# Optimization experiments

Measured on AMD Instinct MI355X. Metric: run time of the kernel, lower is better.

Reference implementation:

```python
import jax, jax.numpy as jnp
import numpy as np

EMB = 300      # emb_size
SEQ = 100      # seq_len
KW = 5         # kernel_width
KN = 50        # kernel_num
KMAX = 3       # maxpooling_num
MLP1 = 75      # decoder_mlp1_num
VOCAB = 50000 + 2
B = 2048
QLEN = 5


def setup_inputs() -> dict:
    key = jax.random.key(0)
    ks = jax.random.split(key, 11)
    input_q = jax.random.randint(ks[0], (QLEN,), 0, 50000)
    input_d = jax.random.randint(ks[1], (B, SEQ), 0, 50000)
    emb_table = jax.random.normal(ks[2], (VOCAB, EMB), jnp.float32) * 0.1
    conv_w = jax.random.normal(ks[3], (KW, 3 * EMB, KN), jnp.float32) * 0.02  # WIO
    conv_b = jnp.zeros((KN,), jnp.float32)
    gate_w = jax.random.normal(ks[4], (EMB, KN), jnp.float32) * 0.05
    gate_b = jnp.zeros((KN,), jnp.float32)
    hid_w = jax.random.normal(ks[5], (KN * KMAX, MLP1), jnp.float32) * 0.05
    hid_b = jnp.zeros((MLP1,), jnp.float32)
    score_w = jax.random.normal(ks[6], (MLP1, 1), jnp.float32) * 0.05
    score_b = jnp.zeros((1,), jnp.float32)
    return {"input_q": input_q, "input_d": input_d, "emb_table": emb_table,
            "conv_w": conv_w, "conv_b": conv_b, "gate_w": gate_w, "gate_b": gate_b,
            "hid_w": hid_w, "hid_b": hid_b, "score_w": score_w, "score_b": score_b}


def kmax_pool(x, k):
    # x: [B, KN, L]; keep top-k values along last axis in original sequence order
    _, idx = jax.lax.top_k(x, k)
    idx = jnp.sort(idx, axis=-1)
    return jnp.take_along_axis(x, idx, axis=-1)  # [B, KN, k]


def reference(input_q, input_d, emb_table, conv_w, conv_b, gate_w, gate_b,
              hid_w, hid_b, score_w, score_b):
    # class vector: mean of query-word embeddings -> [EMB]
    class_vec = emb_table[input_q].mean(axis=0)
    # category-specific gate -> [KN]
    query_gate = jax.nn.sigmoid(class_vec @ gate_w + gate_b)
    # document embeddings -> [B, SEQ, EMB]
    emb = emb_table[input_d]
    # elementwise interaction features, concat -> [B, SEQ, 3*EMB]
    conv_in = jnp.concatenate([emb, class_vec * emb, class_vec - emb], axis=-1)
    # conv over sequence (full-width kernel == 1D conv with C_in=3*EMB) -> [B, SEQ-KW+1, KN]
    conv = jax.lax.conv_general_dilated(
        conv_in, conv_w, window_strides=(1,), padding='VALID',
        dimension_numbers=('NWC', 'WIO', 'NWC')) + conv_b
    gated = query_gate * conv                      # [B, L', KN]
    pooled = kmax_pool(jnp.swapaxes(gated, 1, 2), KMAX)  # [B, KN, KMAX]
    enc = pooled.reshape(pooled.shape[0], -1)      # [B, KN*KMAX] = [B, 150]
    mlp1 = jnp.tanh(enc @ hid_w + hid_b)           # [B, 75]
    score = jnp.tanh(mlp1 @ score_w + score_b)     # [B, 1]
    return (mlp1, score)
```

## Files before the change

### kernel.cpp

```cpp
#include <hip/hip_runtime.h>
#include <math.h>

#define EMB   300
#define SEQ   100
#define KW    5
#define KN    50
#define NPAD  64
#define KMAX  3
#define MLP1  75
#define LOUT  96
#define BATCH 2048
#define EPAD  320
#define CHW   32
#define NCHK  10
#define SROWS 52
#define SPITCHW 36
#define TAU   2.5e-6
#define WHA   0.75
#define WHB   0.25
#define FLAG_TAU 1e-5f

#define WS_C    0
#define WS_GATE 320
#define WS_BIAS 384
#define WS_WG   448
#define F64_DBL 96448
#define WH_F    0
#define WL_F    51200
#define ENC_OFF 102400
#define ENC_PITCH 152
#define FLAGCNT_OFF 413696
#define FLAGLIST_OFF 413704
#define FLAGCAP 4096

typedef __attribute__((ext_vector_type(8))) short short8;
typedef __attribute__((ext_vector_type(4))) float f32x4;

__device__ __forceinline__ unsigned pack_hl(float x) {
    unsigned u = __float_as_uint(x);
    unsigned hi = (u + 0x7fffu + ((u >> 16) & 1u)) >> 16;
    float r = x - __uint_as_float(hi << 16);
    unsigned v = __float_as_uint(r);
    unsigned lo = (v + 0x7fffu + ((v >> 16) & 1u)) >> 16;
    return (hi << 16) | lo;
}

__global__ __launch_bounds__(256) void prep_a(
    const int* __restrict__ qids, const float* __restrict__ emb,
    const float* __restrict__ gate_w, const float* __restrict__ gate_b,
    const float* __restrict__ conv_w, const float* __restrict__ conv_b,
    double* __restrict__ ws, float* wsf)
{
    __shared__ double cS[EMB];
    __shared__ double gS[KN];
    __shared__ double pS[KW][KN];
    int t = threadIdx.x;
    if (t == 0) *(int*)(wsf + FLAGCNT_OFF) = 0;
    for (int e = t; e < EMB; e += 256) {
        double s = 0.0;
        for (int q = 0; q < 5; ++q) s += (double)emb[(size_t)qids[q] * EMB + e];
        double c = s * 0.2;
        cS[e] = c;
        ws[WS_C + e] = c;
    }
    __syncthreads();
    if (t < KN) {
        double g = (double)gate_b[t];
        for (int e = 0; e < EMB; ++e) g += cS[e] * (double)gate_w[e * KN + t];
        g = 1.0 / (1.0 + exp(-g));
        gS[t] = g;
        ws[WS_GATE + t] = g;
    }
    if (t < KW * KN) {
        int n = t % KN, w = t / KN;
        const float* base = conv_w + w * (3 * EMB * KN) + (2 * EMB) * KN + n;
        double p = 0.0;
        for (int e = 0; e < EMB; ++e) p += cS[e] * (double)base[e * KN];
        pS[w][n] = p;
    }
    __syncthreads();
    if (t < KN) {
        double s = (double)conv_b[t];
        for (int w = 0; w < KW; ++w) s += pS[w][t];
        ws[WS_BIAS + t] = gS[t] * s;
    }
}

__global__ __launch_bounds__(256) void prep_b(
    const float* __restrict__ conv_w, const double* __restrict__ ws,
    double* __restrict__ wg, float* __restrict__ wsf)
{
    int gid  = blockIdx.x * 256 + threadIdx.x;
    int wid  = gid >> 6;
    int lane = gid & 63;
    int w = wid / EPAD;
    int e = wid - w * EPAD;
    double v = 0.0;
    if (e < EMB && lane < KN) {
        double c = ws[WS_C + e];
        const float* p = conv_w + (size_t)w * (3 * EMB * KN) + (size_t)e * KN + lane;
        v = ws[WS_GATE + lane] *
            ((double)p[0] + c * (double)p[EMB * KN] - (double)p[2 * EMB * KN]);
    }
    if (e < EMB) wg[(size_t)(w * NPAD + lane) * EMB + e] = v;
    unsigned pk = pack_hl((float)v);
    unsigned short* Wh = (unsigned short*)(wsf + WH_F);
    unsigned short* Wl = (unsigned short*)(wsf + WL_F);
    size_t o = (size_t)(w * NPAD + lane) * EPAD + e;
    Wh[o] = (unsigned short)(pk >> 16);
    Wl[o] = (unsigned short)(pk & 0xffffu);
}

__global__ __launch_bounds__(256, 4) void main_mfma(
    const int* __restrict__ input_d, const float* __restrict__ emb,
    const double* __restrict__ ws, float* wsf,
    const float* __restrict__ hid_w, const float* __restrict__ hid_b,
    const float* __restrict__ score_w, const float* __restrict__ score_b,
    float* __restrict__ out)
{
    __shared__ __align__(16) unsigned stageS[2][2][SROWS][SPITCHW];
    __shared__ int   tokS[4][SROWS];
    __shared__ float encS[2][ENC_PITCH];
    __shared__ float mlpS[2][MLP1 + 1];

    int t = threadIdx.x;
    int wid = t >> 6, lane = t & 63;
    int dl   = wid >> 1;
    int half = wid & 1;
    int bb = blockIdx.x * 2 + dl;
    int m = lane & 15, kg = lane >> 4;

    if (lane < SROWS) tokS[wid][lane] = input_d[bb * SEQ + half * 48 + lane];

    f32x4 acc[3][4];
    #pragma unroll
    for (int lt = 0; lt < 3; ++lt)
        #pragma unroll
        for (int nt = 0; nt < 4; ++nt)
            acc[lt][nt] = (f32x4){0.f, 0.f, 0.f, 0.f};

    const unsigned short* Wh = (const unsigned short*)(wsf + WH_F);
    const unsigned short* Wl = (const unsigned short*)(wsf + WL_F);
    unsigned* stg = &stageS[dl][half][0][0];

    for (int c = 0; c < NCHK; ++c) {
        int e0 = c * CHW;
        #pragma unroll
        for (int it = 0; it < 4; ++it) {
            int i = lane + it * 64;
            if (i < SROWS * 4) {
                int s = i >> 2, eg = i & 3;
                int e = e0 + eg * 8;
                const float* er = emb + (size_t)tokS[wid][s] * EMB;
                float4 fa = {0.f, 0.f, 0.f, 0.f}, fb = {0.f, 0.f, 0.f, 0.f};
                if (e < EMB)     fa = *(const float4*)(er + e);
                if (e + 4 < EMB) fb = *(const float4*)(er + e + 4);
                unsigned p0 = pack_hl(fa.x), p1 = pack_hl(fa.y), p2 = pack_hl(fa.z), p3 = pack_hl(fa.w);
                unsigned p4 = pack_hl(fb.x), p5 = pack_hl(fb.y), p6 = pack_hl(fb.z), p7 = pack_hl(fb.w);
                uint4 hv, lv;
                hv.x = (p0 >> 16)     | (p1 & 0xffff0000u);
                hv.y = (p2 >> 16)     | (p3 & 0xffff0000u);
                hv.z = (p4 >> 16)     | (p5 & 0xffff0000u);
                hv.w = (p6 >> 16)     | (p7 & 0xffff0000u);
                lv.x = (p0 & 0xffffu) | (p1 << 16);
                lv.y = (p2 & 0xffffu) | (p3 << 16);
                lv.z = (p4 & 0xffffu) | (p5 << 16);
                lv.w = (p6 & 0xffffu) | (p7 << 16);
                unsigned* rowp = stg + s * SPITCHW + eg * 8;
                *(uint4*)(rowp)     = hv;
                *(uint4*)(rowp + 4) = lv;
            }
        }
        #pragma unroll 1
        for (int w = 0; w < KW; ++w) {
            short8 Bh[4], Bl[4];
            #pragma unroll
            for (int nt = 0; nt < 4; ++nt) {
                size_t off = (size_t)(w * NPAD + nt * 16 + m) * EPAD + e0 + kg * 8;
                union { uint4 u; short8 s; } xb, yb;
                xb.u = *(const uint4*)(Wh + off);
                yb.u = *(const uint4*)(Wl + off);
                Bh[nt] = xb.s; Bl[nt] = yb.s;
            }
            #pragma unroll
            for (int lt = 0; lt < 3; ++lt) {
                int r = lt * 16 + m + w;
                const unsigned* ap = stg + r * SPITCHW + kg * 8;
                short8 ah = *(const short8*)(ap);
                short8 al = *(const short8*)(ap + 4);
                #pragma unroll
                for (int nt = 0; nt < 4; ++nt) {
                    acc[lt][nt] = __builtin_amdgcn_mfma_f32_16x16x32_bf16(ah, Bh[nt], acc[lt][nt], 0, 0, 0);
                    acc[lt][nt] = __builtin_amdgcn_mfma_f32_16x16x32_bf16(al, Bh[nt], acc[lt][nt], 0, 0, 0);
                    acc[lt][nt] = __builtin_amdgcn_mfma_f32_16x16x32_bf16(ah, Bl[nt], acc[lt][nt], 0, 0, 0);
                }
            }
        }
    }

    __syncthreads();

    float* gated = (float*)&stageS[dl][0][0][0];
    #pragma unroll 1
    for (int ph = 0; ph < 2; ++ph) {
        int np0 = ph * 25;
        #pragma unroll
        for (int nt = 0; nt < 4; ++nt) {
            int n = nt * 16 + m;
            if (n >= np0 && n < np0 + 25) {
                float bias_n = (float)ws[WS_BIAS + n];
                #pragma unroll
                for (int lt = 0; lt < 3; ++lt)
                    #pragma unroll
                    for (int rr = 0; rr < 4; ++rr)
                        gated[(n - np0) * 97 + (half * 3 + lt) * 16 + kg * 4 + rr] = acc[lt][nt][rr] + bias_n;
            }
        }
        __syncthreads();
        int nr = half ? 12 : 13;
        if (lane < nr) {
            int row = half * 13 + lane;
            int n = np0 + row;
            const float* rowp = gated + row * 97;
            float v1 = -1e30f, v2 = -1e30f, v3 = -1e30f, v4 = -1e30f;
            int   i1 = 0, i2 = 0, i3 = 0, i4 = 0;
            for (int l = 0; l < LOUT; ++l) {
                float v = rowp[l];
                if (v > v1)      { v4=v3; i4=i3; v3=v2; i3=i2; v2=v1; i2=i1; v1=v; i1=l; }
                else if (v > v2) { v4=v3; i4=i3; v3=v2; i3=i2; v2=v;  i2=l; }
                else if (v > v3) { v4=v3; i4=i3; v3=v;  i3=l; }
                else if (v > v4) { v4=v;  i4=l; }
            }
            float a0=v1, a1=v2, a2=v3; int j0=i1, j1=i2, j2=i3;
            if (j0 > j1) { float tv=a0; a0=a1; a1=tv; int ti=j0; j0=j1; j1=ti; }
            if (j1 > j2) { float tv=a1; a1=a2; a2=tv; int ti=j1; j1=j2; j2=ti; }
            if (j0 > j1) { float tv=a0; a0=a1; a1=tv; int ti=j0; j0=j1; j1=ti; }
            encS[dl][3*n] = a0; encS[dl][3*n+1] = a1; encS[dl][3*n+2] = a2;
            float* enc = wsf + ENC_OFF + (size_t)bb * ENC_PITCH + 3 * n;
            enc[0] = a0; enc[1] = a1; enc[2] = a2;
            if (v3 - v4 <= FLAG_TAU) {
                int idx = atomicAdd((int*)(wsf + FLAGCNT_OFF), 1);
                if (idx < FLAGCAP) ((int*)(wsf + FLAGLIST_OFF))[idx] = (bb << 6) | n;
            }
        }
        __syncthreads();
    }

    for (int i = t; i < 2 * MLP1; i += 256) {
        int d = i / MLP1, o = i - d * MLP1;
        float h = hid_b[o];
        for (int k = 0; k < KN * KMAX; ++k) h = fmaf(encS[d][k], hid_w[k * MLP1 + o], h);
        h = tanhf(h);
        mlpS[d][o] = h;
        out[(blockIdx.x * 2 + d) * MLP1 + o] = h;
    }
    __syncthreads();
    if (t < 2) {
        float s = score_b[0];
        for (int j = 0; j < MLP1; ++j) s = fmaf(mlpS[t][j], score_w[j], s);
        out[BATCH * MLP1 + blockIdx.x * 2 + t] = tanhf(s);
    }
}

__global__ __launch_bounds__(64) void cleanup_enc(
    const int* __restrict__ input_d, const float* __restrict__ emb,
    const double* __restrict__ ws, float* wsf)
{
    int cnt = *(const int*)(wsf + FLAGCNT_OFF);
    if (cnt > FLAGCAP) cnt = FLAGCAP;
    int idx = blockIdx.x;
    if (idx >= cnt) return;
    int code = ((const int*)(wsf + FLAGLIST_OFF))[idx];
    int b = code >> 6, n = code & 63;
    int lane = threadIdx.x;

    __shared__ int    tokS[SEQ];
    __shared__ double rowS[LOUT];
    for (int i = lane; i < SEQ; i += 64) tokS[i] = input_d[b * SEQ + i];
    __syncthreads();

    for (int l = lane; l < LOUT; l += 64) {
        double s = 0.0;
        for (int w = 0; w < KW; ++w) {
            const float*  er = emb + (size_t)tokS[l + w] * EMB;
            const double* wr = ws + WS_WG + (size_t)(w * NPAD + n) * EMB;
            for (int e = 0; e < EMB; ++e) s += (double)er[e] * wr[e];
        }
        rowS[l] = s + ws[WS_BIAS + n];
    }
    __syncthreads();

    if (lane == 0) {
        double v1=-1e300, v2=-1e300, v3=-1e300, v4=-1e300;
        int    i1=0, i2=0, i3=0, i4=0;
        for (int l = 0; l < LOUT; ++l) {
            double v = rowS[l];
            if (v > v1)      { v4=v3; i4=i3; v3=v2; i3=i2; v2=v1; i2=i1; v1=v; i1=l; }
            else if (v > v2) { v4=v3; i4=i3; v3=v2; i3=i2; v2=v;  i2=l; }
            else if (v > v3) { v4=v3; i4=i3; v3=v;  i3=l; }
            else if (v > v4) { v4=v;  i4=l; }
        }
        double a0=v1, a1=v2, a2=v3; int j0=i1, j1=i2, j2=i3;
        if (j0 > j1) { double tv=a0; a0=a1; a1=tv; int ti=j0; j0=j1; j1=ti; }
        if (j1 > j2) { double tv=a1; a1=a2; a2=tv; int ti=j1; j1=j2; j2=ti; }
        if (j0 > j1) { double tv=a0; a0=a1; a1=tv; int ti=j0; j0=j1; j1=ti; }
        double b0=v1, b1=v2, b2=v4; int k0=i1, k1=i2, k2=i4;
        if (k0 > k1) { double tv=b0; b0=b1; b1=tv; int ti=k0; k0=k1; k1=ti; }
        if (k1 > k2) { double tv=b1; b1=b2; b2=tv; int ti=k1; k1=k2; k2=ti; }
        if (k0 > k1) { double tv=b0; b0=b1; b1=tv; int ti=k0; k0=k1; k1=ti; }
        float* enc = wsf + ENC_OFF + (size_t)b * ENC_PITCH + 3 * n;
        if (v3 - v4 > TAU) {
            enc[0] = (float)a0; enc[1] = (float)a1; enc[2] = (float)a2;
        } else {
            enc[0] = (float)(WHA*a0 + WHB*b0);
            enc[1] = (float)(WHA*a1 + WHB*b1);
            enc[2] = (float)(WHA*a2 + WHB*b2);
        }
    }
}

__global__ __launch_bounds__(128) void cleanup_mlp(
    const float* wsf, const float* __restrict__ hid_w, const float* __restrict__ hid_b,
    const float* __restrict__ score_w, const float* __restrict__ score_b,
    float* __restrict__ out)
{
    int cnt = *(const int*)(wsf + FLAGCNT_OFF);
    if (cnt > FLAGCAP) cnt = FLAGCAP;
    if ((int)blockIdx.x >= cnt) return;
    int code = ((const int*)(wsf + FLAGLIST_OFF))[blockIdx.x];
    int b = code >> 6;
    int t = threadIdx.x;
    __shared__ float eS[KN * KMAX];
    __shared__ float mS[MLP1];
    const float* enc = wsf + ENC_OFF + (size_t)b * ENC_PITCH;
    for (int i = t; i < KN * KMAX; i += 128) eS[i] = enc[i];
    __syncthreads();
    if (t < MLP1) {
        float h = hid_b[t];
        for (int k = 0; k < KN * KMAX; ++k) h = fmaf(eS[k], hid_w[k * MLP1 + t], h);
        h = tanhf(h);
        mS[t] = h;
        out[b * MLP1 + t] = h;
    }
    __syncthreads();
    if (t == 0) {
        float s = score_b[0];
        for (int j = 0; j < MLP1; ++j) s = fmaf(mS[j], score_w[j], s);
        out[BATCH * MLP1 + b] = tanhf(s);
    }
}

extern "C" void kernel_launch(void* const* d_in, const int* in_sizes, int n_in,
                              void* d_out, int out_size, void* d_ws, size_t ws_size,
                              hipStream_t stream)
{
    const int*   input_q = (const int*)d_in[0];
    const int*   input_d = (const int*)d_in[1];
    const float* emb     = (const float*)d_in[2];
    const float* conv_w  = (const float*)d_in[3];
    const float* conv_b  = (const float*)d_in[4];
    const float* gate_w  = (const float*)d_in[5];
    const float* gate_b  = (const float*)d_in[6];
    const float* hid_w   = (const float*)d_in[7];
    const float* hid_b   = (const float*)d_in[8];
    const float* score_w = (const float*)d_in[9];
    const float* score_b = (const float*)d_in[10];
    float*  out = (float*)d_out;
    double* ws  = (double*)d_ws;
    float*  wsf = (float*)((char*)d_ws + (size_t)F64_DBL * 8);

    hipLaunchKernelGGL(prep_a, dim3(1), dim3(256), 0, stream,
                       input_q, emb, gate_w, gate_b, conv_w, conv_b, ws, wsf);
    hipLaunchKernelGGL(prep_b, dim3(400), dim3(256), 0, stream,
                       conv_w, ws, ws + WS_WG, wsf);
    hipLaunchKernelGGL(main_mfma, dim3(BATCH / 2), dim3(256), 0, stream,
                       input_d, emb, ws, wsf, hid_w, hid_b, score_w, score_b, out);
    hipLaunchKernelGGL(cleanup_enc, dim3(FLAGCAP), dim3(64), 0, stream,
                       input_d, emb, ws, wsf);
    hipLaunchKernelGGL(cleanup_mlp, dim3(FLAGCAP), dim3(128), 0, stream,
                       wsf, hid_w, hid_b, score_w, score_b, out);
}
```

Before: 443.1 us.

## Give each wave a full document and prefetch next embedding chunk during MFMA

```diff
diff --git a/kernel.cpp b/kernel.cpp
--- a/kernel.cpp
+++ b/kernel.cpp
@@ -13,8 +13,7 @@
 #define EPAD  320
 #define CHW   32
 #define NCHK  10
-#define SROWS 52
-#define SPITCHW 36
+#define SPW   36
 #define TAU   2.5e-6
 #define WHA   0.75
 #define WHB   0.25
@@ -111,50 +110,63 @@
     Wl[o] = (unsigned short)(pk & 0xffffu);
 }
 
-__global__ __launch_bounds__(256, 4) void main_mfma(
+__global__ __launch_bounds__(256, 2) void main_mfma(
     const int* __restrict__ input_d, const float* __restrict__ emb,
     const double* __restrict__ ws, float* wsf,
     const float* __restrict__ hid_w, const float* __restrict__ hid_b,
     const float* __restrict__ score_w, const float* __restrict__ score_b,
     float* __restrict__ out)
 {
-    __shared__ __align__(16) unsigned stageS[2][2][SROWS][SPITCHW];
-    __shared__ int   tokS[4][SROWS];
-    __shared__ float encS[2][ENC_PITCH];
-    __shared__ float mlpS[2][MLP1 + 1];
+    __shared__ __align__(16) unsigned stageS[4][SEQ * SPW];
+    __shared__ float encS[4][ENC_PITCH];
+    __shared__ float mlpS[4][MLP1 + 1];
 
     int t = threadIdx.x;
     int wid = t >> 6, lane = t & 63;
-    int dl   = wid >> 1;
-    int half = wid & 1;
-    int bb = blockIdx.x * 2 + dl;
+    int bb = blockIdx.x * 4 + wid;
     int m = lane & 15, kg = lane >> 4;
-
-    if (lane < SROWS) tokS[wid][lane] = input_d[bb * SEQ + half * 48 + lane];
-
-    f32x4 acc[3][4];
+    unsigned* stg = &stageS[wid][0];
+
+    int tv[7];
     #pragma unroll
-    for (int lt = 0; lt < 3; ++lt)
+    for (int it = 0; it < 7; ++it) {
+        int i = lane + it * 64;
+        tv[it] = (i < SEQ * 4) ? input_d[bb * SEQ + (i >> 2)] : 0;
+    }
+
+    f32x4 acc[6][4];
+    #pragma unroll
+    for (int lt = 0; lt < 6; ++lt)
         #pragma unroll
         for (int nt = 0; nt < 4; ++nt)
             acc[lt][nt] = (f32x4){0.f, 0.f, 0.f, 0.f};
 
     const unsigned short* Wh = (const unsigned short*)(wsf + WH_F);
     const unsigned short* Wl = (const unsigned short*)(wsf + WL_F);
-    unsigned* stg = &stageS[dl][half][0][0];
-
+
+    float4 pfa[7], pfb[7];
+    #pragma unroll
+    for (int it = 0; it < 7; ++it) {
+        int i = lane + it * 64;
+        float4 z = {0.f, 0.f, 0.f, 0.f};
+        pfa[it] = z; pfb[it] = z;
+        if (i < SEQ * 4) {
+            int eg = i & 3;
+            const float* er = emb + (size_t)tv[it] * EMB + eg * 8;
+            pfa[it] = *(const float4*)(er);
+            pfb[it] = *(const float4*)(er + 4);
+        }
+    }
+
+    #pragma unroll 1
     for (int c = 0; c < NCHK; ++c) {
         int e0 = c * CHW;
         #pragma unroll
-        for (int it = 0; it < 4; ++it) {
+        for (int it = 0; it < 7; ++it) {
             int i = lane + it * 64;
-            if (i < SROWS * 4) {
+            if (i < SEQ * 4) {
                 int s = i >> 2, eg = i & 3;
-                int e = e0 + eg * 8;
-                const float* er = emb + (size_t)tokS[wid][s] * EMB;
-                float4 fa = {0.f, 0.f, 0.f, 0.f}, fb = {0.f, 0.f, 0.f, 0.f};
-                if (e < EMB)     fa = *(const float4*)(er + e);
-                if (e + 4 < EMB) fb = *(const float4*)(er + e + 4);
+                float4 fa = pfa[it], fb = pfb[it];
                 unsigned p0 = pack_hl(fa.x), p1 = pack_hl(fa.y), p2 = pack_hl(fa.z), p3 = pack_hl(fa.w);
                 unsigned p4 = pack_hl(fb.x), p5 = pack_hl(fb.y), p6 = pack_hl(fb.z), p7 = pack_hl(fb.w);
                 uint4 hv, lv;
@@ -166,12 +178,12 @@
                 lv.y = (p2 & 0xffffu) | (p3 << 16);
                 lv.z = (p4 & 0xffffu) | (p5 << 16);
                 lv.w = (p6 & 0xffffu) | (p7 << 16);
-                unsigned* rowp = stg + s * SPITCHW + eg * 8;
+                unsigned* rowp = stg + s * SPW + eg * 8;
                 *(uint4*)(rowp)     = hv;
                 *(uint4*)(rowp + 4) = lv;
             }
         }
-        #pragma unroll 1
+        #pragma unroll
         for (int w = 0; w < KW; ++w) {
             short8 Bh[4], Bl[4];
             #pragma unroll
@@ -182,10 +194,27 @@
                 yb.u = *(const uint4*)(Wl + off);
                 Bh[nt] = xb.s; Bl[nt] = yb.s;
             }
+            if (w == KW - 1 && c + 1 < NCHK) {
+                __builtin_amdgcn_sched_barrier(0);
+                int e0n = e0 + CHW;
+                #pragma unroll
+                for (int it = 0; it < 7; ++it) {
+                    int i = lane + it * 64;
+                    float4 z = {0.f, 0.f, 0.f, 0.f};
+                    pfa[it] = z; pfb[it] = z;
+                    if (i < SEQ * 4) {
+                        int eg = i & 3, e = e0n + eg * 8;
+                        const float* er = emb + (size_t)tv[it] * EMB;
+                        if (e < EMB)     pfa[it] = *(const float4*)(er + e);
+                        if (e + 4 < EMB) pfb[it] = *(const float4*)(er + e + 4);
+                    }
+                }
+                __builtin_amdgcn_sched_barrier(0);
+            }
             #pragma unroll
-            for (int lt = 0; lt < 3; ++lt) {
+            for (int lt = 0; lt < 6; ++lt) {
                 int r = lt * 16 + m + w;
-                const unsigned* ap = stg + r * SPITCHW + kg * 8;
+                const unsigned* ap = stg + r * SPW + kg * 8;
                 short8 ah = *(const short8*)(ap);
                 short8 al = *(const short8*)(ap + 4);
                 #pragma unroll
@@ -198,9 +227,7 @@
         }
     }
 
-    __syncthreads();
-
-    float* gated = (float*)&stageS[dl][0][0][0];
+    float* gated = (float*)stg;
     #pragma unroll 1
     for (int ph = 0; ph < 2; ++ph) {
         int np0 = ph * 25;
@@ -210,18 +237,15 @@
             if (n >= np0 && n < np0 + 25) {
                 float bias_n = (float)ws[WS_BIAS + n];
                 #pragma unroll
-                for (int lt = 0; lt < 3; ++lt)
+                for (int lt = 0; lt < 6; ++lt)
                     #pragma unroll
                     for (int rr = 0; rr < 4; ++rr)
-                        gated[(n - np0) * 97 + (half * 3 + lt) * 16 + kg * 4 + rr] = acc[lt][nt][rr] + bias_n;
-            }
-        }
-        __syncthreads();
-        int nr = half ? 12 : 13;
-        if (lane < nr) {
-            int row = half * 13 + lane;
-            int n = np0 + row;
-            const float* rowp = gated + row * 97;
+                        gated[(n - np0) * 97 + lt * 16 + kg * 4 + rr] = acc[lt][nt][rr] + bias_n;
+            }
+        }
+        if (lane < 25) {
+            int n = np0 + lane;
+            const float* rowp = gated + lane * 97;
             float v1 = -1e30f, v2 = -1e30f, v3 = -1e30f, v4 = -1e30f;
             int   i1 = 0, i2 = 0, i3 = 0, i4 = 0;
             for (int l = 0; l < LOUT; ++l) {
@@ -232,10 +256,10 @@
                 else if (v > v4) { v4=v;  i4=l; }
             }
             float a0=v1, a1=v2, a2=v3; int j0=i1, j1=i2, j2=i3;
-            if (j0 > j1) { float tv=a0; a0=a1; a1=tv; int ti=j0; j0=j1; j1=ti; }
-            if (j1 > j2) { float tv=a1; a1=a2; a2=tv; int ti=j1; j1=j2; j2=ti; }
-            if (j0 > j1) { float tv=a0; a0=a1; a1=tv; int ti=j0; j0=j1; j1=ti; }
-            encS[dl][3*n] = a0; encS[dl][3*n+1] = a1; encS[dl][3*n+2] = a2;
+            if (j0 > j1) { float tv2=a0; a0=a1; a1=tv2; int ti=j0; j0=j1; j1=ti; }
+            if (j1 > j2) { float tv2=a1; a1=a2; a2=tv2; int ti=j1; j1=j2; j2=ti; }
+            if (j0 > j1) { float tv2=a0; a0=a1; a1=tv2; int ti=j0; j0=j1; j1=ti; }
+            encS[wid][3*n] = a0; encS[wid][3*n+1] = a1; encS[wid][3*n+2] = a2;
             float* enc = wsf + ENC_OFF + (size_t)bb * ENC_PITCH + 3 * n;
             enc[0] = a0; enc[1] = a1; enc[2] = a2;
             if (v3 - v4 <= FLAG_TAU) {
@@ -243,22 +267,22 @@
                 if (idx < FLAGCAP) ((int*)(wsf + FLAGLIST_OFF))[idx] = (bb << 6) | n;
             }
         }
-        __syncthreads();
-    }
-
-    for (int i = t; i < 2 * MLP1; i += 256) {
+    }
+    __syncthreads();
+
+    for (int i = t; i < 4 * MLP1; i += 256) {
         int d = i / MLP1, o = i - d * MLP1;
         float h = hid_b[o];
         for (int k = 0; k < KN * KMAX; ++k) h = fmaf(encS[d][k], hid_w[k * MLP1 + o], h);
         h = tanhf(h);
         mlpS[d][o] = h;
-        out[(blockIdx.x * 2 + d) * MLP1 + o] = h;
-    }
-    __syncthreads();
-    if (t < 2) {
+        out[(blockIdx.x * 4 + d) * MLP1 + o] = h;
+    }
+    __syncthreads();
+    if (t < 4) {
         float s = score_b[0];
         for (int j = 0; j < MLP1; ++j) s = fmaf(mlpS[t][j], score_w[j], s);
-        out[BATCH * MLP1 + blockIdx.x * 2 + t] = tanhf(s);
+        out[BATCH * MLP1 + blockIdx.x * 4 + t] = tanhf(s);
     }
 }
 
@@ -373,7 +397,7 @@
                        input_q, emb, gate_w, gate_b, conv_w, conv_b, ws, wsf);
     hipLaunchKernelGGL(prep_b, dim3(400), dim3(256), 0, stream,
                        conv_w, ws, ws + WS_WG, wsf);
-    hipLaunchKernelGGL(main_mfma, dim3(BATCH / 2), dim3(256), 0, stream,
+    hipLaunchKernelGGL(main_mfma, dim3(BATCH / 4), dim3(256), 0, stream,
                        input_d, emb, ws, wsf, hid_w, hid_b, score_w, score_b, out);
     hipLaunchKernelGGL(cleanup_enc, dim3(FLAGCAP), dim3(64), 0, stream,
                        input_d, emb, ws, wsf);
```

New measurement: 404.6 us. 8.7% less time.
